# Kernel tuning notes

Measured on AMD Instinct MI355X. Metric: run time of the kernel, lower is better.

Reference implementation:

```python
import jax, jax.numpy as jnp
import numpy as np

EPS = 1e-8  # torch cosine_similarity default eps


def setup_inputs() -> dict:
    key = jax.random.key(0)
    ks = jax.random.split(key, 10)
    N, W, R = 1048576, 64, 8
    return {
        "memory": jax.random.normal(ks[0], (N, W), dtype=jnp.float32),
        "write_key": jax.random.normal(ks[1], (W,), dtype=jnp.float32),
        "write_strength": jax.random.uniform(ks[2], (1,), dtype=jnp.float32) + 1.0,  # beta in [1, inf)
        "free_gate": jax.random.uniform(ks[3], (R,), dtype=jnp.float32),
        "read_weighting": jax.random.uniform(ks[4], (N, R), dtype=jnp.float32),
        "previous_usage": jax.random.uniform(ks[5], (N,), dtype=jnp.float32),
        "prev_write_weighting": jax.random.uniform(ks[6], (N,), dtype=jnp.float32),
        "allocation_gate": jax.random.uniform(ks[7], (1,), dtype=jnp.float32),
        "write_gate": jax.random.uniform(ks[8], (1,), dtype=jnp.float32),
        "precedence_weighting": jax.random.uniform(ks[9], (N,), dtype=jnp.float32),
    }


def reference(memory, write_key, write_strength, free_gate, read_weighting,
              previous_usage, prev_write_weighting, allocation_gate,
              write_gate, precedence_weighting):
    # --- content weighting: cosine similarity of write_key vs each memory row, scaled, softmax ---
    num = memory @ write_key                                   # (N,)
    denom = jnp.maximum(jnp.linalg.norm(memory, axis=1), EPS) * \
            jnp.maximum(jnp.linalg.norm(write_key), EPS)       # (N,)
    content_w = jax.nn.softmax((num / denom) * write_strength)  # (N,)

    # --- memory retention: phi = prod_r (1 - w_r * f_r) ---
    retention = jnp.prod(1.0 - read_weighting * free_gate, axis=1)  # (N,)

    # --- usage vector recurrence ---
    usage = (previous_usage + prev_write_weighting
             - previous_usage * prev_write_weighting) * retention   # (N,)

    # --- allocation weighting: sort usage ascending, exclusive cumprod, scatter back ---
    order = jnp.argsort(usage)                                  # (N,)
    sorted_u = usage[order]
    excl_cumprod = jnp.concatenate(
        [jnp.ones((1,), sorted_u.dtype), jnp.cumprod(sorted_u)[:-1]])
    alloc = jnp.zeros_like(usage).at[order].set((1.0 - sorted_u) * excl_cumprod)

    # --- gated write weighting ---
    ww = write_gate * (allocation_gate * alloc
                       + (1.0 - allocation_gate) * content_w)   # (N,)

    # --- precedence weighting update ---
    new_precedence = (1.0 - jnp.sum(ww)) * precedence_weighting + ww

    return ww, usage, new_precedence
```

## Files before the change

### kernel.cpp

```cpp
#include <hip/hip_runtime.h>
#include <stdint.h>

#define EPS 1e-8f
#define CAND_CAP 65536u
#define SEL_THREADS 1024
#define SEL_PER 64
#define MAX_SEL 256
#define K_MIN 256u
#define FINF __uint_as_float(0x7f800000u)

__global__ void content_kernel(const float* __restrict__ mem,
                               const float* __restrict__ key,
                               const float* __restrict__ beta_p,
                               float* __restrict__ e_out,
                               float* __restrict__ Zp, int n) {
    __shared__ float skey[64];
    __shared__ float swsum[8];
    int tid = threadIdx.x;
    if (tid < 64) skey[tid] = key[tid];
    __syncthreads();
    float kn = 0.f;
    #pragma unroll
    for (int i = 0; i < 64; ++i) { float v = skey[i]; kn = fmaf(v, v, kn); }
    float scale_k = beta_p[0] / fmaxf(sqrtf(kn), EPS);

    int lane = tid & 63;
    int sub  = lane & 15;
    int rsub = lane >> 4;
    float4 k4 = ((const float4*)skey)[sub];

    long long wave_id     = (long long)((blockIdx.x * blockDim.x + tid) >> 6);
    long long waves_total = (long long)((gridDim.x * blockDim.x) >> 6);
    float zloc = 0.f;
    for (long long row0 = wave_id * 4; row0 < n; row0 += waves_total * 4) {
        long long row = row0 + rsub;
        float4 v = ((const float4*)mem)[row * 16 + sub];
        float d = v.x*k4.x + v.y*k4.y + v.z*k4.z + v.w*k4.w;
        float s = v.x*v.x + v.y*v.y + v.z*v.z + v.w*v.w;
        #pragma unroll
        for (int off = 8; off >= 1; off >>= 1) {
            d += __shfl_xor(d, off, 64);
            s += __shfl_xor(s, off, 64);
        }
        if (sub == 0) {
            float logit = d / fmaxf(sqrtf(s), EPS) * scale_k;
            float e = __expf(logit);
            e_out[row] = e;
            zloc += e;
        }
    }
    #pragma unroll
    for (int off = 32; off >= 1; off >>= 1) zloc += __shfl_xor(zloc, off, 64);
    if (lane == 0) swsum[tid >> 6] = zloc;
    __syncthreads();
    if (tid == 0) {
        float z = 0.f;
        int nw = blockDim.x >> 6;
        for (int i = 0; i < nw; ++i) z += swsum[i];
        atomicAdd(Zp, z);
    }
}

__global__ void usage_kernel(const float* __restrict__ rw,
                             const float* __restrict__ fg,
                             const float* __restrict__ pu,
                             const float* __restrict__ pw,
                             float* __restrict__ us_out,
                             unsigned* __restrict__ hist, int n) {
    __shared__ unsigned lhist[256];
    int tid = threadIdx.x;
    lhist[tid] = 0;
    __syncthreads();
    float f0 = fg[0], f1 = fg[1], f2 = fg[2], f3 = fg[3];
    float f4 = fg[4], f5 = fg[5], f6 = fg[6], f7 = fg[7];
    unsigned big = 0;
    int stride = gridDim.x * blockDim.x;
    for (int i = blockIdx.x * blockDim.x + tid; i < n; i += stride) {
        float4 a = ((const float4*)rw)[i * 2];
        float4 b = ((const float4*)rw)[i * 2 + 1];
        float ret = (1.f - a.x*f0) * (1.f - a.y*f1) * (1.f - a.z*f2) * (1.f - a.w*f3)
                  * (1.f - b.x*f4) * (1.f - b.y*f5) * (1.f - b.z*f6) * (1.f - b.w*f7);
        float u = pu[i], w = pw[i];
        float us = (u + w - u*w) * ret;
        us_out[i] = us;
        unsigned expo = (__float_as_uint(us) >> 23) & 0xffu;
        if (expo >= 120u) big++;
        else atomicAdd(&lhist[expo], 1u);
    }
    if (big) atomicAdd(&lhist[120], big);
    __syncthreads();
    if (lhist[tid]) atomicAdd(&hist[tid], lhist[tid]);
}

__global__ void decide_kernel(const unsigned* __restrict__ hist, float* __restrict__ Tp) {
    unsigned cum = 0;
    int B = 255;
    for (int b = 0; b < 256; ++b) {
        unsigned c = hist[b];
        if (cum + c >= K_MIN) { B = (cum + c <= CAND_CAP) ? b : (b - 1); break; }
        cum += c;
    }
    float T;
    if (B < 0) T = 0.f;
    else if (B >= 254) T = __uint_as_float(0x7f800000u);
    else T = __uint_as_float(((unsigned)(B + 1)) << 23);
    *Tp = T;
}

__global__ void collect_kernel(const float* __restrict__ usage,
                               const float* __restrict__ Tp,
                               float* __restrict__ cand_val,
                               unsigned* __restrict__ cand_idx,
                               unsigned* __restrict__ counter, int n) {
    float T = *Tp;
    int stride = gridDim.x * blockDim.x;
    for (int i = blockIdx.x * blockDim.x + threadIdx.x; i < n; i += stride) {
        float u = usage[i];
        if (u < T) {
            unsigned p = atomicAdd(counter, 1u);
            if (p < CAND_CAP) { cand_val[p] = u; cand_idx[p] = i; }
        }
    }
}

__global__ __launch_bounds__(SEL_THREADS)
void select_kernel(const float* __restrict__ cand_val,
                   const unsigned* __restrict__ cand_idx,
                   const unsigned* __restrict__ counter,
                   unsigned* __restrict__ sel_idx,
                   float* __restrict__ sel_alloc,
                   float* __restrict__ Sap,
                   unsigned* __restrict__ selcnt) {
    __shared__ float    wmin[SEL_THREADS / 64];
    __shared__ unsigned wpos[SEL_THREADS / 64];
    __shared__ float    bminS;
    __shared__ unsigned bposS;
    int tid = threadIdx.x;
    unsigned C = *counter; if (C > CAND_CAP) C = CAND_CAP;
    float v[SEL_PER];
    #pragma unroll
    for (int j = 0; j < SEL_PER; ++j) {
        unsigned p = (unsigned)(j * SEL_THREADS + tid);
        v[j] = (p < C) ? cand_val[p] : FINF;
    }
    float P = 1.f, Sa = 0.f;
    unsigned nsel = 0;
    for (int k = 0; k < MAX_SEL; ++k) {
        float lv = FINF;
        unsigned lpos = 0xffffffffu;
        #pragma unroll
        for (int j = 0; j < SEL_PER; ++j)
            if (v[j] < lv) { lv = v[j]; lpos = (unsigned)(j * SEL_THREADS + tid); }
        #pragma unroll
        for (int off = 32; off >= 1; off >>= 1) {
            float ov = __shfl_xor(lv, off, 64);
            unsigned op = __shfl_xor(lpos, off, 64);
            if (ov < lv) { lv = ov; lpos = op; }
        }
        if ((tid & 63) == 0) { wmin[tid >> 6] = lv; wpos[tid >> 6] = lpos; }
        __syncthreads();
        if (tid == 0) {
            float gm = wmin[0]; unsigned gp = wpos[0];
            #pragma unroll
            for (int i = 1; i < SEL_THREADS / 64; ++i)
                if (wmin[i] < gm) { gm = wmin[i]; gp = wpos[i]; }
            bminS = gm; bposS = gp;
        }
        __syncthreads();
        float gm = bminS; unsigned gp = bposS;
        if (!(gm < FINF) || P < 1e-38f) break;
        float a = (1.f - gm) * P;
        Sa += a; P *= gm; nsel++;
        if (tid == 0) { sel_alloc[k] = a; sel_idx[k] = cand_idx[gp]; }
        if ((gp & (unsigned)(SEL_THREADS - 1)) == (unsigned)tid) {
            unsigned jj = gp / SEL_THREADS;
            #pragma unroll
            for (int j = 0; j < SEL_PER; ++j)
                if ((unsigned)j == jj) v[j] = FINF;
        }
    }
    if (tid == 0) { *Sap = Sa; *selcnt = nsel; }
}

__global__ void final_kernel(const float* __restrict__ e,
                             const float* __restrict__ prec,
                             const float* __restrict__ Zp,
                             const float* __restrict__ Sap,
                             const float* __restrict__ wg_p,
                             const float* __restrict__ ag_p,
                             float* __restrict__ out_ww,
                             float* __restrict__ out_prec, int n) {
    float Z = *Zp, Sa = *Sap, wg = *wg_p, ag = *ag_p;
    float cscale = wg * (1.f - ag) / Z;
    float om = 1.f - wg * (ag * Sa + (1.f - ag));
    int stride = gridDim.x * blockDim.x;
    for (int i = blockIdx.x * blockDim.x + threadIdx.x; i < n; i += stride) {
        float wwc = cscale * e[i];
        out_ww[i] = wwc;
        out_prec[i] = om * prec[i] + wwc;
    }
}

__global__ void scatter_kernel(const unsigned* __restrict__ sel_idx,
                               const float* __restrict__ sel_alloc,
                               const unsigned* __restrict__ selcnt,
                               const float* __restrict__ wg_p,
                               const float* __restrict__ ag_p,
                               float* __restrict__ out_ww,
                               float* __restrict__ out_prec) {
    unsigned c = *selcnt;
    float coef = wg_p[0] * ag_p[0];
    unsigned t = threadIdx.x;
    if (t < c) {
        unsigned idx = sel_idx[t];
        float add = coef * sel_alloc[t];
        out_ww[idx] += add;
        out_prec[idx] += add;
    }
}

extern "C" void kernel_launch(void* const* d_in, const int* in_sizes, int n_in,
                              void* d_out, int out_size, void* d_ws, size_t ws_size,
                              hipStream_t stream) {
    const float* memory = (const float*)d_in[0];
    const float* wkey   = (const float*)d_in[1];
    const float* beta   = (const float*)d_in[2];
    const float* fgate  = (const float*)d_in[3];
    const float* rw     = (const float*)d_in[4];
    const float* pu     = (const float*)d_in[5];
    const float* pww    = (const float*)d_in[6];
    const float* agate  = (const float*)d_in[7];
    const float* wgate  = (const float*)d_in[8];
    const float* prec   = (const float*)d_in[9];
    int n = in_sizes[5];

    float* out_ww = (float*)d_out;
    float* out_us = out_ww + n;
    float* out_pr = out_ww + 2 * (size_t)n;

    char* ws = (char*)d_ws;
    float* e_buf = (float*)ws;
    char* ctrl = ws + (size_t)n * 4;
    float*    Zp       = (float*)(ctrl + 0);
    unsigned* counter  = (unsigned*)(ctrl + 4);
    float*    Tp       = (float*)(ctrl + 8);
    unsigned* selcnt   = (unsigned*)(ctrl + 12);
    float*    Sap      = (float*)(ctrl + 16);
    unsigned* hist     = (unsigned*)(ctrl + 32);
    unsigned* sel_idx  = (unsigned*)(ctrl + 32 + 1024);
    float*    sel_all  = (float*)(ctrl + 32 + 2048);
    float*    cand_val = (float*)(ctrl + 4096);
    unsigned* cand_idx = (unsigned*)(ctrl + 4096 + CAND_CAP * 4);

    hipMemsetAsync(ctrl, 0, 4096, stream);

    content_kernel<<<4096, 256, 0, stream>>>(memory, wkey, beta, e_buf, Zp, n);
    usage_kernel<<<2048, 256, 0, stream>>>(rw, fgate, pu, pww, out_us, hist, n);
    decide_kernel<<<1, 1, 0, stream>>>(hist, Tp);
    collect_kernel<<<1024, 256, 0, stream>>>(out_us, Tp, cand_val, cand_idx, counter, n);
    select_kernel<<<1, SEL_THREADS, 0, stream>>>(cand_val, cand_idx, counter,
                                                 sel_idx, sel_all, Sap, selcnt);
    final_kernel<<<2048, 256, 0, stream>>>(e_buf, prec, Zp, Sap, wgate, agate,
                                           out_ww, out_pr, n);
    scatter_kernel<<<1, MAX_SEL, 0, stream>>>(sel_idx, sel_all, selcnt, wgate, agate,
                                              out_ww, out_pr);
}
```

Baseline: 510.4 us.

## Fuse seven-kernel pipeline into three kernels and derive precedence scale algebraically

Result: faster. 488.4 us (-4.3%).

```diff
diff --git a/kernel.cpp b/kernel.cpp
--- a/kernel.cpp
+++ b/kernel.cpp
@@ -9,16 +9,26 @@
 #define K_MIN 256u
 #define FINF __uint_as_float(0x7f800000u)
 
-__global__ void content_kernel(const float* __restrict__ mem,
-                               const float* __restrict__ key,
-                               const float* __restrict__ beta_p,
-                               float* __restrict__ e_out,
-                               float* __restrict__ Zp, int n) {
+__global__ __launch_bounds__(256)
+void k1_content_usage(const float* __restrict__ mem,
+                      const float* __restrict__ key,
+                      const float* __restrict__ beta_p,
+                      const float* __restrict__ rw,
+                      const float* __restrict__ fg,
+                      const float* __restrict__ pu,
+                      const float* __restrict__ pw,
+                      float* __restrict__ e_out,
+                      float* __restrict__ us_out,
+                      float* __restrict__ Zp,
+                      unsigned* __restrict__ hist, int n) {
     __shared__ float skey[64];
-    __shared__ float swsum[8];
+    __shared__ float swsum[4];
+    __shared__ unsigned lhist[256];
     int tid = threadIdx.x;
     if (tid < 64) skey[tid] = key[tid];
-    __syncthreads();
+    lhist[tid] = 0;
+    __syncthreads();
+
     float kn = 0.f;
     #pragma unroll
     for (int i = 0; i < 64; ++i) { float v = skey[i]; kn = fmaf(v, v, kn); }
@@ -29,11 +39,11 @@
     int rsub = lane >> 4;
     float4 k4 = ((const float4*)skey)[sub];
 
-    long long wave_id     = (long long)((blockIdx.x * blockDim.x + tid) >> 6);
-    long long waves_total = (long long)((gridDim.x * blockDim.x) >> 6);
+    int wave_id     = (blockIdx.x * 256 + tid) >> 6;
+    int waves_total = (gridDim.x * 256) >> 6;
     float zloc = 0.f;
-    for (long long row0 = wave_id * 4; row0 < n; row0 += waves_total * 4) {
-        long long row = row0 + rsub;
+    for (int row0 = wave_id * 4; row0 < n; row0 += waves_total * 4) {
+        int row = row0 + rsub;
         float4 v = ((const float4*)mem)[row * 16 + sub];
         float d = v.x*k4.x + v.y*k4.y + v.z*k4.z + v.w*k4.w;
         float s = v.x*v.x + v.y*v.y + v.z*v.z + v.w*v.w;
@@ -52,30 +62,12 @@
     #pragma unroll
     for (int off = 32; off >= 1; off >>= 1) zloc += __shfl_xor(zloc, off, 64);
     if (lane == 0) swsum[tid >> 6] = zloc;
-    __syncthreads();
-    if (tid == 0) {
-        float z = 0.f;
-        int nw = blockDim.x >> 6;
-        for (int i = 0; i < nw; ++i) z += swsum[i];
-        atomicAdd(Zp, z);
-    }
-}
-
-__global__ void usage_kernel(const float* __restrict__ rw,
-                             const float* __restrict__ fg,
-                             const float* __restrict__ pu,
-                             const float* __restrict__ pw,
-                             float* __restrict__ us_out,
-                             unsigned* __restrict__ hist, int n) {
-    __shared__ unsigned lhist[256];
-    int tid = threadIdx.x;
-    lhist[tid] = 0;
-    __syncthreads();
+
     float f0 = fg[0], f1 = fg[1], f2 = fg[2], f3 = fg[3];
     float f4 = fg[4], f5 = fg[5], f6 = fg[6], f7 = fg[7];
     unsigned big = 0;
-    int stride = gridDim.x * blockDim.x;
-    for (int i = blockIdx.x * blockDim.x + tid; i < n; i += stride) {
+    int stride = gridDim.x * 256;
+    for (int i = blockIdx.x * 256 + tid; i < n; i += stride) {
         float4 a = ((const float4*)rw)[i * 2];
         float4 b = ((const float4*)rw)[i * 2 + 1];
         float ret = (1.f - a.x*f0) * (1.f - a.y*f1) * (1.f - a.z*f2) * (1.f - a.w*f3)
@@ -89,52 +81,83 @@
     }
     if (big) atomicAdd(&lhist[120], big);
     __syncthreads();
-    if (lhist[tid]) atomicAdd(&hist[tid], lhist[tid]);
-}
-
-__global__ void decide_kernel(const unsigned* __restrict__ hist, float* __restrict__ Tp) {
-    unsigned cum = 0;
-    int B = 255;
-    for (int b = 0; b < 256; ++b) {
-        unsigned c = hist[b];
-        if (cum + c >= K_MIN) { B = (cum + c <= CAND_CAP) ? b : (b - 1); break; }
-        cum += c;
-    }
-    float T;
-    if (B < 0) T = 0.f;
-    else if (B >= 254) T = __uint_as_float(0x7f800000u);
-    else T = __uint_as_float(((unsigned)(B + 1)) << 23);
-    *Tp = T;
-}
-
-__global__ void collect_kernel(const float* __restrict__ usage,
-                               const float* __restrict__ Tp,
-                               float* __restrict__ cand_val,
-                               unsigned* __restrict__ cand_idx,
-                               unsigned* __restrict__ counter, int n) {
-    float T = *Tp;
-    int stride = gridDim.x * blockDim.x;
-    for (int i = blockIdx.x * blockDim.x + threadIdx.x; i < n; i += stride) {
-        float u = usage[i];
-        if (u < T) {
-            unsigned p = atomicAdd(counter, 1u);
-            if (p < CAND_CAP) { cand_val[p] = u; cand_idx[p] = i; }
-        }
+    if (tid == 0) {
+        atomicAdd(Zp, swsum[0] + swsum[1] + swsum[2] + swsum[3]);
+    }
+    unsigned c = lhist[tid];
+    if (c) atomicAdd(&hist[tid], c);
+}
+
+__global__ __launch_bounds__(256)
+void k2_final_collect(const float* __restrict__ e,
+                      const float* __restrict__ prec,
+                      const float* __restrict__ usage,
+                      const unsigned* __restrict__ hist,
+                      const float* __restrict__ Zp,
+                      const float* __restrict__ wg_p,
+                      const float* __restrict__ ag_p,
+                      float* __restrict__ out_ww,
+                      float* __restrict__ out_prec,
+                      float* __restrict__ cand_val,
+                      unsigned* __restrict__ cand_idx,
+                      unsigned* __restrict__ counter, int n4) {
+    __shared__ unsigned shist[256];
+    __shared__ float sT;
+    int tid = threadIdx.x;
+    shist[tid] = hist[tid];
+    __syncthreads();
+    if (tid == 0) {
+        unsigned cum = 0; int B = 255;
+        for (int b = 0; b < 256; ++b) {
+            unsigned c = shist[b];
+            if (cum + c >= K_MIN) { B = (cum + c <= CAND_CAP) ? b : (b - 1); break; }
+            cum += c;
+        }
+        float T;
+        if (B < 0) T = 0.f;
+        else if (B >= 254) T = FINF;
+        else T = __uint_as_float(((unsigned)(B + 1)) << 23);
+        sT = T;
+    }
+    __syncthreads();
+    float T = sT;
+    float Z = *Zp, wg = *wg_p, ag = *ag_p;
+    float cscale = wg * (1.f - ag) / Z;
+    float om = 1.f - wg;
+    int stride = gridDim.x * 256;
+    for (int i = blockIdx.x * 256 + tid; i < n4; i += stride) {
+        float4 ev = ((const float4*)e)[i];
+        float4 pv = ((const float4*)prec)[i];
+        float4 uv = ((const float4*)usage)[i];
+        float4 ww, pr;
+        ww.x = cscale * ev.x; ww.y = cscale * ev.y;
+        ww.z = cscale * ev.z; ww.w = cscale * ev.w;
+        pr.x = om * pv.x + ww.x; pr.y = om * pv.y + ww.y;
+        pr.z = om * pv.z + ww.z; pr.w = om * pv.w + ww.w;
+        ((float4*)out_ww)[i] = ww;
+        ((float4*)out_prec)[i] = pr;
+        int base = i * 4;
+        if (uv.x < T) { unsigned p = atomicAdd(counter, 1u); if (p < CAND_CAP) { cand_val[p] = uv.x; cand_idx[p] = base; } }
+        if (uv.y < T) { unsigned p = atomicAdd(counter, 1u); if (p < CAND_CAP) { cand_val[p] = uv.y; cand_idx[p] = base + 1; } }
+        if (uv.z < T) { unsigned p = atomicAdd(counter, 1u); if (p < CAND_CAP) { cand_val[p] = uv.z; cand_idx[p] = base + 2; } }
+        if (uv.w < T) { unsigned p = atomicAdd(counter, 1u); if (p < CAND_CAP) { cand_val[p] = uv.w; cand_idx[p] = base + 3; } }
     }
 }
 
 __global__ __launch_bounds__(SEL_THREADS)
-void select_kernel(const float* __restrict__ cand_val,
-                   const unsigned* __restrict__ cand_idx,
-                   const unsigned* __restrict__ counter,
-                   unsigned* __restrict__ sel_idx,
-                   float* __restrict__ sel_alloc,
-                   float* __restrict__ Sap,
-                   unsigned* __restrict__ selcnt) {
+void k3_select_scatter(const float* __restrict__ cand_val,
+                       const unsigned* __restrict__ cand_idx,
+                       const unsigned* __restrict__ counter,
+                       const float* __restrict__ wg_p,
+                       const float* __restrict__ ag_p,
+                       float* __restrict__ out_ww,
+                       float* __restrict__ out_prec) {
     __shared__ float    wmin[SEL_THREADS / 64];
     __shared__ unsigned wpos[SEL_THREADS / 64];
     __shared__ float    bminS;
     __shared__ unsigned bposS;
+    __shared__ float    s_alloc[MAX_SEL];
+    __shared__ unsigned s_idx[MAX_SEL];
     int tid = threadIdx.x;
     unsigned C = *counter; if (C > CAND_CAP) C = CAND_CAP;
     float v[SEL_PER];
@@ -143,7 +166,7 @@
         unsigned p = (unsigned)(j * SEL_THREADS + tid);
         v[j] = (p < C) ? cand_val[p] : FINF;
     }
-    float P = 1.f, Sa = 0.f;
+    float P = 1.f;
     unsigned nsel = 0;
     for (int k = 0; k < MAX_SEL; ++k) {
         float lv = FINF;
@@ -169,9 +192,8 @@
         __syncthreads();
         float gm = bminS; unsigned gp = bposS;
         if (!(gm < FINF) || P < 1e-38f) break;
-        float a = (1.f - gm) * P;
-        Sa += a; P *= gm; nsel++;
-        if (tid == 0) { sel_alloc[k] = a; sel_idx[k] = cand_idx[gp]; }
+        if (tid == 0) { s_alloc[k] = (1.f - gm) * P; s_idx[k] = cand_idx[gp]; }
+        P *= gm; nsel++;
         if ((gp & (unsigned)(SEL_THREADS - 1)) == (unsigned)tid) {
             unsigned jj = gp / SEL_THREADS;
             #pragma unroll
@@ -179,42 +201,12 @@
                 if ((unsigned)j == jj) v[j] = FINF;
         }
     }
-    if (tid == 0) { *Sap = Sa; *selcnt = nsel; }
-}
-
-__global__ void final_kernel(const float* __restrict__ e,
-                             const float* __restrict__ prec,
-                             const float* __restrict__ Zp,
-                             const float* __restrict__ Sap,
-                             const float* __restrict__ wg_p,
-                             const float* __restrict__ ag_p,
-                             float* __restrict__ out_ww,
-                             float* __restrict__ out_prec, int n) {
-    float Z = *Zp, Sa = *Sap, wg = *wg_p, ag = *ag_p;
-    float cscale = wg * (1.f - ag) / Z;
-    float om = 1.f - wg * (ag * Sa + (1.f - ag));
-    int stride = gridDim.x * blockDim.x;
-    for (int i = blockIdx.x * blockDim.x + threadIdx.x; i < n; i += stride) {
-        float wwc = cscale * e[i];
-        out_ww[i] = wwc;
-        out_prec[i] = om * prec[i] + wwc;
-    }
-}
-
-__global__ void scatter_kernel(const unsigned* __restrict__ sel_idx,
-                               const float* __restrict__ sel_alloc,
-                               const unsigned* __restrict__ selcnt,
-                               const float* __restrict__ wg_p,
-                               const float* __restrict__ ag_p,
-                               float* __restrict__ out_ww,
-                               float* __restrict__ out_prec) {
-    unsigned c = *selcnt;
+    __syncthreads();
     float coef = wg_p[0] * ag_p[0];
-    unsigned t = threadIdx.x;
-    if (t < c) {
-        unsigned idx = sel_idx[t];
-        float add = coef * sel_alloc[t];
-        out_ww[idx] += add;
+    if ((unsigned)tid < nsel) {
+        unsigned idx = s_idx[tid];
+        float add = coef * s_alloc[tid];
+        out_ww[idx]   += add;
         out_prec[idx] += add;
     }
 }
@@ -243,25 +235,17 @@
     char* ctrl = ws + (size_t)n * 4;
     float*    Zp       = (float*)(ctrl + 0);
     unsigned* counter  = (unsigned*)(ctrl + 4);
-    float*    Tp       = (float*)(ctrl + 8);
-    unsigned* selcnt   = (unsigned*)(ctrl + 12);
-    float*    Sap      = (float*)(ctrl + 16);
     unsigned* hist     = (unsigned*)(ctrl + 32);
-    unsigned* sel_idx  = (unsigned*)(ctrl + 32 + 1024);
-    float*    sel_all  = (float*)(ctrl + 32 + 2048);
     float*    cand_val = (float*)(ctrl + 4096);
     unsigned* cand_idx = (unsigned*)(ctrl + 4096 + CAND_CAP * 4);
 
     hipMemsetAsync(ctrl, 0, 4096, stream);
 
-    content_kernel<<<4096, 256, 0, stream>>>(memory, wkey, beta, e_buf, Zp, n);
-    usage_kernel<<<2048, 256, 0, stream>>>(rw, fgate, pu, pww, out_us, hist, n);
-    decide_kernel<<<1, 1, 0, stream>>>(hist, Tp);
-    collect_kernel<<<1024, 256, 0, stream>>>(out_us, Tp, cand_val, cand_idx, counter, n);
-    select_kernel<<<1, SEL_THREADS, 0, stream>>>(cand_val, cand_idx, counter,
-                                                 sel_idx, sel_all, Sap, selcnt);
-    final_kernel<<<2048, 256, 0, stream>>>(e_buf, prec, Zp, Sap, wgate, agate,
-                                           out_ww, out_pr, n);
-    scatter_kernel<<<1, MAX_SEL, 0, stream>>>(sel_idx, sel_all, selcnt, wgate, agate,
-                                              out_ww, out_pr);
-}
+    k1_content_usage<<<2048, 256, 0, stream>>>(memory, wkey, beta, rw, fgate, pu, pww,
+                                               e_buf, out_us, Zp, hist, n);
+    k2_final_collect<<<1024, 256, 0, stream>>>(e_buf, prec, out_us, hist, Zp, wgate, agate,
+                                               out_ww, out_pr, cand_val, cand_idx, counter,
+                                               n / 4);
+    k3_select_scatter<<<1, SEL_THREADS, 0, stream>>>(cand_val, cand_idx, counter,
+                                                     wgate, agate, out_ww, out_pr);
+}
```
